# Optimization experiments

Hardware: AMD Instinct MI355X
Metric: run time of the kernel (lower is better)

The kernel has to match this reference:

```python
import jax, jax.numpy as jnp
import numpy as np

N_NODES = 50000
N_EDGES = 800000
N_REL = 6
N_LAYERS = 8
D = 256
NUM_GRAPHS = 512


def setup_inputs() -> dict:
    key = jax.random.key(0)
    ks = jax.random.split(key, 24)
    s = lambda *sh: 1.0 / np.sqrt(sh[0])
    inp = {
        "x": jax.random.normal(ks[0], (N_NODES, 13), dtype=jnp.float32),
        "edge_index": jax.random.randint(ks[1], (2, N_EDGES), 0, N_NODES, dtype=jnp.int64),
        "edge_type": jax.random.randint(ks[2], (N_EDGES,), 0, N_REL, dtype=jnp.int64),
        "batch": jnp.sort(jax.random.randint(ks[3], (N_NODES,), 0, NUM_GRAPHS, dtype=jnp.int64)),
        "enc_W": jax.random.normal(ks[4], (13, D), dtype=jnp.float32) * s(13),
        "enc_b": jnp.zeros((D,), dtype=jnp.float32),
        "prelu_a": jnp.float32(0.25),
        "rel_W": jax.random.normal(ks[5], (N_LAYERS, N_REL, D, D), dtype=jnp.float32) * s(D),
        "root_W": jax.random.normal(ks[6], (N_LAYERS, D, D), dtype=jnp.float32) * s(D),
        "conv_b": jnp.zeros((N_LAYERS, D), dtype=jnp.float32),
        "gp_W1": jax.random.normal(ks[7], (D, D), dtype=jnp.float32) * s(D),
        "gp_b1": jnp.zeros((D,), dtype=jnp.float32),
        "gp_W2": jax.random.normal(ks[8], (D, D), dtype=jnp.float32) * s(D),
        "gp_b2": jnp.zeros((D,), dtype=jnp.float32),
        "fc_W1": jax.random.normal(ks[9], (D, 1024), dtype=jnp.float32) * s(D),
        "fc_b1": jnp.zeros((1024,), dtype=jnp.float32),
        "fc_W2": jax.random.normal(ks[10], (1024, 512), dtype=jnp.float32) * s(1024),
        "fc_b2": jnp.zeros((512,), dtype=jnp.float32),
        "out_W": jax.random.normal(ks[11], (512, 1), dtype=jnp.float32) * s(512),
        "out_b": jnp.zeros((1,), dtype=jnp.float32),
    }
    return inp


def reference(x, edge_index, edge_type, batch, enc_W, enc_b, prelu_a, rel_W, root_W,
              conv_b, gp_W1, gp_b1, gp_W2, gp_b2, fc_W1, fc_b1, fc_W2, fc_b2, out_W, out_b):
    src, dst = edge_index[0], edge_index[1]
    h = x @ enc_W + enc_b  # [N, D]
    for i in range(N_LAYERS):
        skip = h
        # per-relation transform for all nodes: [R, N, D]
        xW = jnp.einsum('nd,rde->rne', h, rel_W[i])
        msgs = xW[edge_type, src]  # [E, D] gather by (relation, source node)
        agg = jax.ops.segment_sum(msgs, dst, num_segments=N_NODES)
        h = agg + h @ root_W[i] + conv_b[i]
        h = h + skip
        h = jnp.where(h > 0, h, prelu_a * h)  # PReLU (shared scalar)
        norm = jnp.sqrt(jnp.sum(h * h, axis=1, keepdims=True))
        h = h / jnp.maximum(norm, 1e-12)  # F.normalize(p=2, dim=1)
    g = jax.nn.relu(h @ gp_W1 + gp_b1) @ gp_W2 + gp_b2
    pooled = jax.ops.segment_sum(g, batch, num_segments=NUM_GRAPHS)  # global_add_pool
    z = jax.nn.relu(pooled @ fc_W1 + fc_b1)  # dropout = identity at eval
    z = jax.nn.relu(z @ fc_W2 + fc_b2)
    return jax.nn.relu(z @ out_W + out_b)  # [NUM_GRAPHS, 1]
```

## Files before the change

kernel.cpp:

```cpp
#include <hip/hip_runtime.h>

#define N_NODES   50000
#define N_EDGES   800000
#define N_REL     6
#define N_LAYERS  8
#define DD        256
#define NUM_GRAPHS 512

#define NKEYS      (N_REL * N_NODES)
#define SCAN_T     256
#define SCAN_E     8
#define SCAN_CHUNK (SCAN_T * SCAN_E)
#define SCAN_NB    ((NKEYS + SCAN_CHUNK - 1) / SCAN_CHUNK)

typedef _Float16 h4 __attribute__((ext_vector_type(4)));
typedef _Float16 h8 __attribute__((ext_vector_type(8)));
typedef float    f4 __attribute__((ext_vector_type(4)));

__device__ __forceinline__ void atomAddF(float* p, float v) { unsafeAtomicAdd(p, v); }

__device__ __forceinline__ void load_lds16(const void* g, void* l) {
    __builtin_amdgcn_global_load_lds(
        (const __attribute__((address_space(1))) uint32_t*)g,
        (__attribute__((address_space(3))) uint32_t*)l, 16, 0, 0);
}

__global__ __launch_bounds__(256) void enc_kernel(const float* __restrict__ x,
                                                  const float* __restrict__ W,
                                                  const float* __restrict__ b,
                                                  _Float16* __restrict__ Hhi,
                                                  _Float16* __restrict__ Hlo) {
    int n = blockIdx.x;
    int d = threadIdx.x;
    float s = b[d];
#pragma unroll
    for (int k = 0; k < 13; ++k) s = fmaf(x[n * 13 + k], W[k * 256 + d], s);
    const _Float16 hi = (_Float16)s;
    Hhi[(size_t)n * DD + d] = hi;
    Hlo[(size_t)n * DD + d] = (_Float16)(s - (float)hi);
}

__global__ __launch_bounds__(256) void wsplit_rel_kernel(const float* __restrict__ relW,
                                                         const float* __restrict__ rootW,
                                                         _Float16* __restrict__ wthi,
                                                         _Float16* __restrict__ wtlo) {
    const size_t id = (size_t)blockIdx.x * 256 + threadIdx.x;
    if (id >= (size_t)N_LAYERS * 7 * 256 * 256) return;
    const int k = (int)(id & 255);
    const int n = (int)((id >> 8) & 255);
    const int g = (int)((id >> 16) % 7);
    const int L = (int)((id >> 16) / 7);
    float w = (g < 6)
        ? relW[(((size_t)L * 6 + g) * 256 + k) * 256 + n]
        : rootW[((size_t)L * 256 + k) * 256 + n];
    if (g == 6 && k == n) w += 1.0f;
    const _Float16 hi = (_Float16)w;
    const size_t o = ((size_t)L * 256 + n) * 1792 + (size_t)g * 256 + k;
    wthi[o] = hi;
    wtlo[o] = (_Float16)(w - (float)hi);
}

__global__ __launch_bounds__(256) void wsplit_tr_kernel(const float* __restrict__ W,
                                                        _Float16* __restrict__ whi,
                                                        _Float16* __restrict__ wlo,
                                                        int K, int N) {
    const size_t id = (size_t)blockIdx.x * 256 + threadIdx.x;
    if (id >= (size_t)K * N) return;
    const int k = (int)(id % K), n = (int)(id / K);
    const float w = W[(size_t)k * N + n];
    const _Float16 hi = (_Float16)w;
    whi[(size_t)n * K + k] = hi;
    wlo[(size_t)n * K + k] = (_Float16)(w - (float)hi);
}

__global__ __launch_bounds__(256) void fsplit_kernel(const float* __restrict__ S,
                                                     _Float16* __restrict__ hi,
                                                     _Float16* __restrict__ lo, int total) {
    const int id = blockIdx.x * 256 + threadIdx.x;
    if (id >= total) return;
    const float v = S[id];
    const _Float16 h = (_Float16)v;
    hi[id] = h;
    lo[id] = (_Float16)(v - (float)h);
}

template <int MODE>
__global__ __launch_bounds__(256, 2) void gemm_lds(
    const _Float16* __restrict__ Ahi, const _Float16* __restrict__ Alo,
    const _Float16* __restrict__ Hhi, const _Float16* __restrict__ Hlo,
    const _Float16* __restrict__ Bhi, const _Float16* __restrict__ Blo,
    int lda, int ldb, int ldc, int boff_agg, int boff_h, int K_agg, int K_tot,
    float* __restrict__ Cf, _Float16* __restrict__ Ohi, _Float16* __restrict__ Olo,
    const float* __restrict__ bias, const float* __restrict__ pa, int M) {
    __shared__ _Float16 smem[24576];
    const int lane = threadIdx.x & 63;
    const int wave = threadIdx.x >> 6;
    const int lm = lane & 15, lq = lane >> 4;
    const int wm = wave & 1, wn = wave >> 1;
    const int mb = blockIdx.x * 128;
    const int nb = blockIdx.y * 256;

    f4 acc[4][8];
#pragma unroll
    for (int i = 0; i < 4; ++i)
#pragma unroll
        for (int j = 0; j < 8; ++j) acc[i][j] = (f4){0.f, 0.f, 0.f, 0.f};

    for (int k0 = 0; k0 < K_tot; k0 += 32) {
        const _Float16 *pAh, *pAl;
        int acol, bcol;
        if (k0 < K_agg) {
            const size_t pb = (size_t)(k0 >> 8) * (size_t)N_NODES * DD;
            pAh = Ahi + pb; pAl = Alo + pb;
            acol = k0 & 255;
            bcol = boff_agg + k0;
        } else {
            pAh = Hhi; pAl = Hlo;
            acol = k0 - K_agg;
            bcol = boff_h + (k0 - K_agg);
        }

        __syncthreads();
#pragma unroll
        for (int q = 0; q < 12; ++q) {
            const int ub = (q * 4 + wave) * 64;
            const int u  = ub + lane;
            const _Float16* gp;
            size_t ga;
            if (q < 4) {
                const int v = u & 511, row = v >> 2, slot = v & 3;
                const int c = slot ^ ((row >> 1) & 3);
                int rg = mb + row; if (rg >= M) rg = M - 1;
                gp = (q < 2) ? pAh : pAl;
                ga = (size_t)rg * lda + acol + c * 8;
            } else {
                const int v = u & 1023, row = v >> 2, slot = v & 3;
                const int c = slot ^ ((row >> 1) & 3);
                gp = (q < 8) ? Bhi : Blo;
                ga = (size_t)(nb + row) * ldb + bcol + c * 8;
            }
            load_lds16(gp + ga, smem + (size_t)ub * 8);
        }
        __syncthreads();

        h8 ah[4], al[4], bh[8], bl[8];
#pragma unroll
        for (int i = 0; i < 4; ++i) {
            const int row  = wm * 64 + i * 16 + lm;
            const int slot = lq ^ ((row >> 1) & 3);
            const int o    = (row * 4 + slot) * 8;
            ah[i] = *(const h8*)(smem + o);
            al[i] = *(const h8*)(smem + 4096 + o);
        }
#pragma unroll
        for (int j = 0; j < 8; ++j) {
            const int n    = wn * 128 + j * 16 + lm;
            const int slot = lq ^ ((n >> 1) & 3);
            const int o    = (n * 4 + slot) * 8;
            bh[j] = *(const h8*)(smem + 8192 + o);
            bl[j] = *(const h8*)(smem + 16384 + o);
        }
#pragma unroll
        for (int i = 0; i < 4; ++i)
#pragma unroll
            for (int j = 0; j < 8; ++j) {
                acc[i][j] = __builtin_amdgcn_mfma_f32_16x16x32_f16(ah[i], bh[j], acc[i][j], 0, 0, 0);
                acc[i][j] = __builtin_amdgcn_mfma_f32_16x16x32_f16(ah[i], bl[j], acc[i][j], 0, 0, 0);
                acc[i][j] = __builtin_amdgcn_mfma_f32_16x16x32_f16(al[i], bh[j], acc[i][j], 0, 0, 0);
            }
    }

    if (MODE == 0) {
#pragma unroll
        for (int i = 0; i < 4; ++i)
#pragma unroll
            for (int r = 0; r < 4; ++r) {
                const int row = mb + wm * 64 + i * 16 + lq * 4 + r;
                if (row >= M) continue;
#pragma unroll
                for (int j = 0; j < 8; ++j) {
                    const int col = nb + wn * 128 + j * 16 + lm;
                    Cf[(size_t)row * ldc + col] = acc[i][j][r] + bias[col];
                }
            }
    } else if (MODE == 3) {
#pragma unroll
        for (int i = 0; i < 4; ++i)
#pragma unroll
            for (int r = 0; r < 4; ++r) {
                const int row = mb + wm * 64 + i * 16 + lq * 4 + r;
                if (row >= M) continue;
#pragma unroll
                for (int j = 0; j < 8; ++j) {
                    const int col = nb + wn * 128 + j * 16 + lm;
                    Cf[(size_t)row * ldc + col] += acc[i][j][r];
                }
            }
    } else if (MODE == 2 || MODE == 4) {
#pragma unroll
        for (int i = 0; i < 4; ++i)
#pragma unroll
            for (int r = 0; r < 4; ++r) {
                const int row = mb + wm * 64 + i * 16 + lq * 4 + r;
                if (row >= M) continue;
#pragma unroll
                for (int j = 0; j < 8; ++j) {
                    const int col = nb + wn * 128 + j * 16 + lm;
                    float v = acc[i][j][r] + bias[col];
                    if (MODE == 2) v = fmaxf(v, 0.f);
                    const _Float16 hi = (_Float16)v;
                    const size_t idx = (size_t)row * ldc + col;
                    Ohi[idx] = hi;
                    Olo[idx] = (_Float16)(v - (float)hi);
                }
            }
    } else {
        float* shf = (float*)smem;
        const float a = pa[0];
        __syncthreads();
#pragma unroll
        for (int i = 0; i < 4; ++i)
#pragma unroll
            for (int r = 0; r < 4; ++r) {
                const int rl  = i * 16 + lq * 4 + r;
                const int row = mb + wm * 64 + rl;
                float rss = 0.f;
                if (row < M) {
#pragma unroll
                    for (int j = 0; j < 8; ++j) {
                        const int col = nb + wn * 128 + j * 16 + lm;
                        float v = acc[i][j][r] + Cf[(size_t)row * ldc + col];
                        v = v > 0.f ? v : a * v;
                        acc[i][j][r] = v;
                        rss = fmaf(v, v, rss);
                    }
                }
                rss += __shfl_xor(rss, 1, 64);
                rss += __shfl_xor(rss, 2, 64);
                rss += __shfl_xor(rss, 4, 64);
                rss += __shfl_xor(rss, 8, 64);
                if (lm == 0 && row < M) shf[wave * 64 + rl] = rss;
            }
        __syncthreads();
#pragma unroll
        for (int i = 0; i < 4; ++i)
#pragma unroll
            for (int r = 0; r < 4; ++r) {
                const int rl  = i * 16 + lq * 4 + r;
                const int row = mb + wm * 64 + rl;
                if (row >= M) continue;
                const float tot = shf[wm * 64 + rl] + shf[(2 + wm) * 64 + rl];
                const float inv = 1.0f / fmaxf(sqrtf(tot), 1e-12f);
#pragma unroll
                for (int j = 0; j < 8; ++j) {
                    const int col = nb + wn * 128 + j * 16 + lm;
                    const float v = acc[i][j][r] * inv;
                    const _Float16 hi = (_Float16)v;
                    const size_t idx = (size_t)row * ldc + col;
                    Ohi[idx] = hi;
                    Olo[idx] = (_Float16)(v - (float)hi);
                }
            }
    }
}

__global__ __launch_bounds__(256) void hist_kernel(const int* __restrict__ dst,
                                                   const int* __restrict__ etype,
                                                   int* __restrict__ cnt) {
    const int e = blockIdx.x * 256 + threadIdx.x;
    if (e >= N_EDGES) return;
    atomicAdd(&cnt[etype[e] * N_NODES + dst[e]], 1);
}

__global__ __launch_bounds__(SCAN_T) void scan1_kernel(const int* __restrict__ cnt,
                                                       int* __restrict__ off,
                                                       int* __restrict__ bsum) {
    __shared__ int sh[SCAN_T];
    const int b = blockIdx.x, t = threadIdx.x;
    const int base = b * SCAN_CHUNK + t * SCAN_E;
    int pre[SCAN_E];
    int s = 0;
#pragma unroll
    for (int i = 0; i < SCAN_E; ++i) {
        const int x = (base + i < NKEYS) ? cnt[base + i] : 0;
        pre[i] = s;
        s += x;
    }
    sh[t] = s;
    __syncthreads();
    for (int d = 1; d < SCAN_T; d <<= 1) {
        const int x = (t >= d) ? sh[t - d] : 0;
        __syncthreads();
        sh[t] += x;
        __syncthreads();
    }
    const int toff = (t == 0) ? 0 : sh[t - 1];
#pragma unroll
    for (int i = 0; i < SCAN_E; ++i)
        if (base + i < NKEYS) off[base + i] = toff + pre[i];
    if (t == SCAN_T - 1) bsum[b] = sh[SCAN_T - 1];
}

__global__ __launch_bounds__(SCAN_T) void scan2_kernel(int* __restrict__ bsum, int n) {
    __shared__ int sh[SCAN_T];
    const int t = threadIdx.x;
    const int base = t * SCAN_E;
    int pre[SCAN_E];
    int s = 0;
#pragma unroll
    for (int i = 0; i < SCAN_E; ++i) {
        const int x = (base + i < n) ? bsum[base + i] : 0;
        pre[i] = s;
        s += x;
    }
    sh[t] = s;
    __syncthreads();
    for (int d = 1; d < SCAN_T; d <<= 1) {
        const int x = (t >= d) ? sh[t - d] : 0;
        __syncthreads();
        sh[t] += x;
        __syncthreads();
    }
    const int toff = (t == 0) ? 0 : sh[t - 1];
#pragma unroll
    for (int i = 0; i < SCAN_E; ++i)
        if (base + i < n) bsum[base + i] = toff + pre[i];
}

__global__ __launch_bounds__(SCAN_T) void scan3_kernel(int* __restrict__ off,
                                                       const int* __restrict__ bsum) {
    const int b = blockIdx.x, t = threadIdx.x;
    const int add = bsum[b];
    const int base = b * SCAN_CHUNK + t * SCAN_E;
#pragma unroll
    for (int i = 0; i < SCAN_E; ++i)
        if (base + i < NKEYS) off[base + i] += add;
    if (b == 0 && t == 0) off[NKEYS] = N_EDGES;
}

__global__ __launch_bounds__(256) void csr_fill_kernel(const int* __restrict__ src,
                                                       const int* __restrict__ dst,
                                                       const int* __restrict__ etype,
                                                       int* __restrict__ cursor,
                                                       int* __restrict__ sorted_src) {
    const int e = blockIdx.x * 256 + threadIdx.x;
    if (e >= N_EDGES) return;
    const int key = etype[e] * N_NODES + dst[e];
    const int pos = atomicAdd(&cursor[key], 1);
    sorted_src[pos] = src[e];
}

__global__ __launch_bounds__(256) void agg_kernel(const _Float16* __restrict__ Hhi,
                                                  const _Float16* __restrict__ Hlo,
                                                  const int* __restrict__ off,
                                                  const int* __restrict__ isrc,
                                                  _Float16* __restrict__ agghi,
                                                  _Float16* __restrict__ agglo,
                                                  int rel0, int nrel) {
    const int p    = blockIdx.x * 4 + (threadIdx.x >> 6);
    const int lane = threadIdx.x & 63;
    const int half = lane >> 5, li = lane & 31;
    if (p >= nrel * N_NODES) return;
    const int pl   = p / N_NODES;
    const int node = p - pl * N_NODES;
    const int r    = rel0 + pl;
    const int s0 = off[r * N_NODES + node];
    const int s1 = off[r * N_NODES + node + 1];
    float a[8] = {0.f, 0.f, 0.f, 0.f, 0.f, 0.f, 0.f, 0.f};
    for (int e0 = s0; e0 < s1; e0 += 4) {
        const int ea = e0 + half;
        const int eb = e0 + 2 + half;
        const int sa = (ea < s1) ? isrc[ea] : -1;
        const int sb = (eb < s1) ? isrc[eb] : -1;
        if (sa >= 0) {
            const h8 vh = *(const h8*)(Hhi + (size_t)sa * DD + li * 8);
            const h8 vl = *(const h8*)(Hlo + (size_t)sa * DD + li * 8);
#pragma unroll
            for (int k = 0; k < 8; ++k) a[k] += (float)vh[k] + (float)vl[k];
        }
        if (sb >= 0) {
            const h8 vh = *(const h8*)(Hhi + (size_t)sb * DD + li * 8);
            const h8 vl = *(const h8*)(Hlo + (size_t)sb * DD + li * 8);
#pragma unroll
            for (int k = 0; k < 8; ++k) a[k] += (float)vh[k] + (float)vl[k];
        }
    }
#pragma unroll
    for (int k = 0; k < 8; ++k) a[k] += __shfl_xor(a[k], 32, 64);
    if (half == 0) {
        h8 oh, ol;
#pragma unroll
        for (int k = 0; k < 8; ++k) {
            oh[k] = (_Float16)a[k];
            ol[k] = (_Float16)(a[k] - (float)oh[k]);
        }
        const size_t o = ((size_t)pl * N_NODES + node) * DD + li * 8;
        *(h8*)(agghi + o) = oh;
        *(h8*)(agglo + o) = ol;
    }
}

__global__ __launch_bounds__(64) void pool_kernel(const _Float16* __restrict__ ghi,
                                                  const _Float16* __restrict__ glo,
                                                  const int* __restrict__ batch,
                                                  float* __restrict__ pooled) {
    const int c     = threadIdx.x;
    const int start = blockIdx.x * 128;
    const int end   = min(start + 128, N_NODES);
    int cur = batch[start];
    float4 acc = {0.f, 0.f, 0.f, 0.f};
    for (int n = start; n < end; ++n) {
        const int bn = batch[n];
        if (bn != cur) {
            float* p = pooled + (size_t)cur * DD + c * 4;
            atomAddF(p + 0, acc.x); atomAddF(p + 1, acc.y);
            atomAddF(p + 2, acc.z); atomAddF(p + 3, acc.w);
            acc = {0.f, 0.f, 0.f, 0.f};
            cur = bn;
        }
        const h4 vh = *(const h4*)(ghi + (size_t)n * DD + c * 4);
        const h4 vl = *(const h4*)(glo + (size_t)n * DD + c * 4);
        acc.x += (float)vh[0] + (float)vl[0];
        acc.y += (float)vh[1] + (float)vl[1];
        acc.z += (float)vh[2] + (float)vl[2];
        acc.w += (float)vh[3] + (float)vl[3];
    }
    float* p = pooled + (size_t)cur * DD + c * 4;
    atomAddF(p + 0, acc.x); atomAddF(p + 1, acc.y);
    atomAddF(p + 2, acc.z); atomAddF(p + 3, acc.w);
}

__global__ __launch_bounds__(64) void out_kernel(const _Float16* __restrict__ z2hi,
                                                 const _Float16* __restrict__ z2lo,
                                                 const float* __restrict__ W,
                                                 const float* __restrict__ b,
                                                 float* __restrict__ out) {
    const int g = blockIdx.x;
    const int t = threadIdx.x;
    float s = 0.f;
#pragma unroll
    for (int j = 0; j < 8; ++j) {
        const int idx = t + 64 * j;
        const float z = (float)z2hi[(size_t)g * 512 + idx] + (float)z2lo[(size_t)g * 512 + idx];
        s = fmaf(z, W[idx], s);
    }
#pragma unroll
    for (int off = 32; off; off >>= 1) s += __shfl_xor(s, off, 64);
    if (t == 0) {
        const float v = s + b[0];
        out[g] = v > 0.f ? v : 0.f;
    }
}

extern "C" void kernel_launch(void* const* d_in, const int* in_sizes, int n_in,
                              void* d_out, int out_size, void* d_ws, size_t ws_size,
                              hipStream_t stream) {
    const float* x       = (const float*)d_in[0];
    const int*   eidx    = (const int*)d_in[1];
    const int*   etype   = (const int*)d_in[2];
    const int*   batch   = (const int*)d_in[3];
    const float* enc_W   = (const float*)d_in[4];
    const float* enc_b   = (const float*)d_in[5];
    const float* prelu_a = (const float*)d_in[6];
    const float* rel_W   = (const float*)d_in[7];
    const float* root_W  = (const float*)d_in[8];
    const float* conv_b  = (const float*)d_in[9];
    const float* gp_W1   = (const float*)d_in[10];
    const float* gp_b1   = (const float*)d_in[11];
    const float* gp_W2   = (const float*)d_in[12];
    const float* gp_b2   = (const float*)d_in[13];
    const float* fc_W1   = (const float*)d_in[14];
    const float* fc_b1   = (const float*)d_in[15];
    const float* fc_W2   = (const float*)d_in[16];
    const float* fc_b2   = (const float*)d_in[17];
    const float* out_W   = (const float*)d_in[18];
    const float* out_b   = (const float*)d_in[19];
    float* out = (float*)d_out;

    uint8_t* wp = (uint8_t*)d_ws;
    auto alloc = [&](size_t bytes) {
        void* r = (void*)wp;
        wp += (bytes + 255) & ~(size_t)255;
        return r;
    };
    float*    base   = (float*)alloc((size_t)N_NODES * DD * 4);
    _Float16* Hhi    = (_Float16*)alloc((size_t)N_NODES * DD * 2);
    _Float16* Hlo    = (_Float16*)alloc((size_t)N_NODES * DD * 2);
    _Float16* agghi  = (_Float16*)alloc((size_t)2 * N_NODES * DD * 2);
    _Float16* agglo  = (_Float16*)alloc((size_t)2 * N_NODES * DD * 2);
    _Float16* wthi   = (_Float16*)alloc((size_t)N_LAYERS * 256 * 1792 * 2);
    _Float16* wtlo   = (_Float16*)alloc((size_t)N_LAYERS * 256 * 1792 * 2);
    _Float16* wtg1hi = (_Float16*)alloc((size_t)256 * 256 * 2);
    _Float16* wtg1lo = (_Float16*)alloc((size_t)256 * 256 * 2);
    _Float16* wtg2hi = (_Float16*)alloc((size_t)256 * 256 * 2);
    _Float16* wtg2lo = (_Float16*)alloc((size_t)256 * 256 * 2);
    _Float16* wtf1hi = (_Float16*)alloc((size_t)1024 * 256 * 2);
    _Float16* wtf1lo = (_Float16*)alloc((size_t)1024 * 256 * 2);
    _Float16* wtf2hi = (_Float16*)alloc((size_t)512 * 1024 * 2);
    _Float16* wtf2lo = (_Float16*)alloc((size_t)512 * 1024 * 2);
    float*    pooled = (float*)alloc((size_t)NUM_GRAPHS * DD * 4);
    _Float16* phi    = (_Float16*)alloc((size_t)NUM_GRAPHS * DD * 2);
    _Float16* plo    = (_Float16*)alloc((size_t)NUM_GRAPHS * DD * 2);
    _Float16* z1hi   = (_Float16*)alloc((size_t)NUM_GRAPHS * 1024 * 2);
    _Float16* z1lo   = (_Float16*)alloc((size_t)NUM_GRAPHS * 1024 * 2);
    _Float16* z2hi   = (_Float16*)alloc((size_t)NUM_GRAPHS * 512 * 2);
    _Float16* z2lo   = (_Float16*)alloc((size_t)NUM_GRAPHS * 512 * 2);
    int*      ioff   = (int*)alloc((size_t)(NKEYS + 1) * 4);
    int*      icur   = (int*)alloc((size_t)NKEYS * 4);
    int*      ibsum  = (int*)alloc(256 * 4);
    int*      isrc   = (int*)alloc((size_t)N_EDGES * 4);

    const int* src = eidx;
    const int* dst = eidx + N_EDGES;

    const size_t wtot = (size_t)N_LAYERS * 7 * 256 * 256;
    wsplit_rel_kernel<<<(int)((wtot + 255) / 256), 256, 0, stream>>>(rel_W, root_W, wthi, wtlo);
    wsplit_tr_kernel<<<256, 256, 0, stream>>>(gp_W1, wtg1hi, wtg1lo, 256, 256);
    wsplit_tr_kernel<<<256, 256, 0, stream>>>(gp_W2, wtg2hi, wtg2lo, 256, 256);
    wsplit_tr_kernel<<<1024, 256, 0, stream>>>(fc_W1, wtf1hi, wtf1lo, 256, 1024);
    wsplit_tr_kernel<<<2048, 256, 0, stream>>>(fc_W2, wtf2hi, wtf2lo, 1024, 512);

    hipMemsetAsync(icur, 0, (size_t)NKEYS * sizeof(int), stream);
    const int eb = (N_EDGES + 255) / 256;
    hist_kernel<<<eb, 256, 0, stream>>>(dst, etype, icur);
    scan1_kernel<<<SCAN_NB, SCAN_T, 0, stream>>>(icur, ioff, ibsum);
    scan2_kernel<<<1, SCAN_T, 0, stream>>>(ibsum, SCAN_NB);
    scan3_kernel<<<SCAN_NB, SCAN_T, 0, stream>>>(ioff, ibsum);
    hipMemcpyAsync(icur, ioff, (size_t)NKEYS * sizeof(int), hipMemcpyDeviceToDevice, stream);
    csr_fill_kernel<<<eb, 256, 0, stream>>>(src, dst, etype, icur, isrc);

    enc_kernel<<<N_NODES, 256, 0, stream>>>(x, enc_W, enc_b, Hhi, Hlo);

    const dim3 gG((N_NODES + 127) / 128, 1);
    const int  aggb = (2 * N_NODES + 3) / 4;

    for (int L = 0; L < N_LAYERS; ++L) {
        const _Float16* Bh = wthi + (size_t)L * 256 * 1792;
        const _Float16* Bl = wtlo + (size_t)L * 256 * 1792;
        agg_kernel<<<aggb, 256, 0, stream>>>(Hhi, Hlo, ioff, isrc, agghi, agglo, 0, 2);
        gemm_lds<0><<<gG, 256, 0, stream>>>(agghi, agglo, Hhi, Hlo, Bh, Bl,
                                            256, 1792, 256, 0, 1536, 512, 768,
                                            base, nullptr, nullptr,
                                            conv_b + L * DD, nullptr, N_NODES);
        agg_kernel<<<aggb, 256, 0, stream>>>(Hhi, Hlo, ioff, isrc, agghi, agglo, 2, 2);
        gemm_lds<3><<<gG, 256, 0, stream>>>(agghi, agglo, nullptr, nullptr, Bh, Bl,
                                            256, 1792, 256, 512, 0, 512, 512,
                                            base, nullptr, nullptr,
                                            nullptr, nullptr, N_NODES);
        agg_kernel<<<aggb, 256, 0, stream>>>(Hhi, Hlo, ioff, isrc, agghi, agglo, 4, 2);
        gemm_lds<1><<<gG, 256, 0, stream>>>(agghi, agglo, nullptr, nullptr, Bh, Bl,
                                            256, 1792, 256, 1024, 0, 512, 512,
                                            base, Hhi, Hlo,
                                            nullptr, prelu_a, N_NODES);
    }

    gemm_lds<2><<<gG, 256, 0, stream>>>(nullptr, nullptr, Hhi, Hlo, wtg1hi, wtg1lo,
                                        256, 256, 256, 0, 0, 0, 256,
                                        nullptr, agghi, agglo, gp_b1, nullptr, N_NODES);
    gemm_lds<4><<<gG, 256, 0, stream>>>(agghi, agglo, nullptr, nullptr, wtg2hi, wtg2lo,
                                        256, 256, 256, 0, 0, 256, 256,
                                        nullptr, agghi + (size_t)N_NODES * DD,
                                        agglo + (size_t)N_NODES * DD, gp_b2, nullptr, N_NODES);

    hipMemsetAsync(pooled, 0, (size_t)NUM_GRAPHS * DD * sizeof(float), stream);
    pool_kernel<<<(N_NODES + 127) / 128, 64, 0, stream>>>(
        agghi + (size_t)N_NODES * DD, agglo + (size_t)N_NODES * DD, batch, pooled);
    fsplit_kernel<<<(NUM_GRAPHS * DD + 255) / 256, 256, 0, stream>>>(
        pooled, phi, plo, NUM_GRAPHS * DD);

    gemm_lds<2><<<dim3(4, 4), 256, 0, stream>>>(nullptr, nullptr, phi, plo, wtf1hi, wtf1lo,
                                                256, 256, 1024, 0, 0, 0, 256,
                                                nullptr, z1hi, z1lo, fc_b1, nullptr,
                                                NUM_GRAPHS);
    gemm_lds<2><<<dim3(4, 2), 256, 0, stream>>>(nullptr, nullptr, z1hi, z1lo, wtf2hi, wtf2lo,
                                                1024, 1024, 512, 0, 0, 0, 1024,
                                                nullptr, z2hi, z2lo, fc_b2, nullptr,
                                                NUM_GRAPHS);
    out_kernel<<<NUM_GRAPHS, 64, 0, stream>>>(z2hi, z2lo, out_W, out_b, out);
}
```

Baseline: 3.225 ms.

## Fuse neighbor aggregation into per-layer GEMM kernel

Replaces the three aggregate-then-GEMM pairs per layer with a single layer kernel. Each block gathers relation-wise neighbor sums for its 128 nodes directly into shared memory, then runs the MFMA GEMM plus the PReLU/normalize epilogue. This removes the intermediate aggregation buffers, the fp32 partial-sum round trips and most launches. In exchange, the edge list is re-read for every 32-column chunk and the gathers are serialized per thread with no overlap against the matrix work.

```diff
diff --git a/kernel.cpp b/kernel.cpp
--- a/kernel.cpp
+++ b/kernel.cpp
@@ -84,14 +84,194 @@
     lo[id] = (_Float16)(v - (float)h);
 }
 
+__global__ __launch_bounds__(256, 2) void layer_kernel(
+    const _Float16* __restrict__ Hhi, const _Float16* __restrict__ Hlo,
+    const _Float16* __restrict__ Bhi, const _Float16* __restrict__ Blo,
+    const int* __restrict__ ioff, const int* __restrict__ isrc,
+    _Float16* __restrict__ Hnhi, _Float16* __restrict__ Hnlo,
+    const float* __restrict__ bias, const float* __restrict__ pa) {
+    __shared__ _Float16 smem[24576];
+    const int tid  = threadIdx.x;
+    const int lane = tid & 63;
+    const int wave = tid >> 6;
+    const int lm = lane & 15, lq = lane >> 4;
+    const int wm = wave & 1, wn = wave >> 1;
+    const int mb = blockIdx.x * 128;
+
+    const int nl   = tid >> 1;
+    const int half = tid & 1;
+    const int node = min(mb + nl, N_NODES - 1);
+
+    f4 acc[4][8];
+#pragma unroll
+    for (int i = 0; i < 4; ++i)
+#pragma unroll
+        for (int j = 0; j < 8; ++j) acc[i][j] = (f4){0.f, 0.f, 0.f, 0.f};
+
+    for (int seg = 0; seg < 7; ++seg) {
+        const bool isrel = (seg < 6);
+        int s0 = 0, s1 = 0;
+        if (isrel) {
+            s0 = ioff[seg * N_NODES + node];
+            s1 = ioff[seg * N_NODES + node + 1];
+        }
+#pragma unroll 1
+        for (int c8 = 0; c8 < 8; ++c8) {
+            const int acol = c8 * 32;
+            const int bcol = seg * 256 + acol;
+
+            __syncthreads();
+
+            if (isrel) {
+                float afp[16];
+#pragma unroll
+                for (int j = 0; j < 16; ++j) afp[j] = 0.f;
+                const int dbase = acol + half * 16;
+                for (int e = s0; e < s1; ++e) {
+                    const int s = isrc[e];
+                    const size_t hb = (size_t)s * DD + dbase;
+                    const h8 vh0 = *(const h8*)(Hhi + hb);
+                    const h8 vh1 = *(const h8*)(Hhi + hb + 8);
+                    const h8 vl0 = *(const h8*)(Hlo + hb);
+                    const h8 vl1 = *(const h8*)(Hlo + hb + 8);
+#pragma unroll
+                    for (int j = 0; j < 8; ++j) {
+                        afp[j]     += (float)vh0[j] + (float)vl0[j];
+                        afp[8 + j] += (float)vh1[j] + (float)vl1[j];
+                    }
+                }
+#pragma unroll
+                for (int u = 0; u < 2; ++u) {
+                    h8 oh, ol;
+#pragma unroll
+                    for (int j = 0; j < 8; ++j) {
+                        const float v = afp[u * 8 + j];
+                        oh[j] = (_Float16)v;
+                        ol[j] = (_Float16)(v - (float)oh[j]);
+                    }
+                    const int cc   = half * 2 + u;
+                    const int slot = cc ^ ((nl >> 1) & 3);
+                    const int o    = (nl * 4 + slot) * 8;
+                    *(h8*)(smem + o)        = oh;
+                    *(h8*)(smem + 4096 + o) = ol;
+                }
+#pragma unroll
+                for (int q = 4; q < 12; ++q) {
+                    const int ub = (q * 4 + wave) * 64;
+                    const int u  = (ub + lane) & 1023;
+                    const int row = u >> 2, slot = u & 3;
+                    const int cx = slot ^ ((row >> 1) & 3);
+                    const _Float16* gp = (q < 8) ? Bhi : Blo;
+                    const size_t gb = (size_t)row * 1792 + bcol + cx * 8;
+                    load_lds16(gp + gb, smem + (size_t)ub * 8);
+                }
+            } else {
+#pragma unroll
+                for (int q = 0; q < 12; ++q) {
+                    const int ub = (q * 4 + wave) * 64;
+                    const int u  = ub + lane;
+                    const _Float16* gp;
+                    size_t ga;
+                    if (q < 4) {
+                        const int v = u & 511, row = v >> 2, slot = v & 3;
+                        const int cx = slot ^ ((row >> 1) & 3);
+                        const int rg = min(mb + row, N_NODES - 1);
+                        gp = (q < 2) ? Hhi : Hlo;
+                        ga = (size_t)rg * DD + acol + cx * 8;
+                    } else {
+                        const int v = u & 1023, row = v >> 2, slot = v & 3;
+                        const int cx = slot ^ ((row >> 1) & 3);
+                        gp = (q < 8) ? Bhi : Blo;
+                        ga = (size_t)row * 1792 + bcol + cx * 8;
+                    }
+                    load_lds16(gp + ga, smem + (size_t)ub * 8);
+                }
+            }
+            __syncthreads();
+
+            h8 ah[4], al[4], bh[8], bl[8];
+#pragma unroll
+            for (int i = 0; i < 4; ++i) {
+                const int row  = wm * 64 + i * 16 + lm;
+                const int slot = lq ^ ((row >> 1) & 3);
+                const int o    = (row * 4 + slot) * 8;
+                ah[i] = *(const h8*)(smem + o);
+                al[i] = *(const h8*)(smem + 4096 + o);
+            }
+#pragma unroll
+            for (int j = 0; j < 8; ++j) {
+                const int n    = wn * 128 + j * 16 + lm;
+                const int slot = lq ^ ((n >> 1) & 3);
+                const int o    = (n * 4 + slot) * 8;
+                bh[j] = *(const h8*)(smem + 8192 + o);
+                bl[j] = *(const h8*)(smem + 16384 + o);
+            }
+#pragma unroll
+            for (int i = 0; i < 4; ++i)
+#pragma unroll
+                for (int j = 0; j < 8; ++j) {
+                    acc[i][j] = __builtin_amdgcn_mfma_f32_16x16x32_f16(ah[i], bh[j], acc[i][j], 0, 0, 0);
+                    acc[i][j] = __builtin_amdgcn_mfma_f32_16x16x32_f16(ah[i], bl[j], acc[i][j], 0, 0, 0);
+                    acc[i][j] = __builtin_amdgcn_mfma_f32_16x16x32_f16(al[i], bh[j], acc[i][j], 0, 0, 0);
+                }
+        }
+    }
+
+    float* shf = (float*)smem;
+    const float a = pa[0];
+    __syncthreads();
+#pragma unroll
+    for (int i = 0; i < 4; ++i)
+#pragma unroll
+        for (int r = 0; r < 4; ++r) {
+            const int rl  = i * 16 + lq * 4 + r;
+            const int row = mb + wm * 64 + rl;
+            float rss = 0.f;
+            if (row < N_NODES) {
+#pragma unroll
+                for (int j = 0; j < 8; ++j) {
+                    const int col = wn * 128 + j * 16 + lm;
+                    float v = acc[i][j][r] + bias[col];
+                    v = v > 0.f ? v : a * v;
+                    acc[i][j][r] = v;
+                    rss = fmaf(v, v, rss);
+                }
+            }
+            rss += __shfl_xor(rss, 1, 64);
+            rss += __shfl_xor(rss, 2, 64);
+            rss += __shfl_xor(rss, 4, 64);
+            rss += __shfl_xor(rss, 8, 64);
+            if (lm == 0 && row < N_NODES) shf[wave * 64 + rl] = rss;
+        }
+    __syncthreads();
+#pragma unroll
+    for (int i = 0; i < 4; ++i)
+#pragma unroll
+        for (int r = 0; r < 4; ++r) {
+            const int rl  = i * 16 + lq * 4 + r;
+            const int row = mb + wm * 64 + rl;
+            if (row >= N_NODES) continue;
+            const float tot = shf[wm * 64 + rl] + shf[(2 + wm) * 64 + rl];
+            const float inv = 1.0f / fmaxf(sqrtf(tot), 1e-12f);
+#pragma unroll
+            for (int j = 0; j < 8; ++j) {
+                const int col = wn * 128 + j * 16 + lm;
+                const float v = acc[i][j][r] * inv;
+                const _Float16 hi = (_Float16)v;
+                const size_t idx = (size_t)row * DD + col;
+                Hnhi[idx] = hi;
+                Hnlo[idx] = (_Float16)(v - (float)hi);
+            }
+        }
+}
+
 template <int MODE>
 __global__ __launch_bounds__(256, 2) void gemm_lds(
     const _Float16* __restrict__ Ahi, const _Float16* __restrict__ Alo,
-    const _Float16* __restrict__ Hhi, const _Float16* __restrict__ Hlo,
     const _Float16* __restrict__ Bhi, const _Float16* __restrict__ Blo,
-    int lda, int ldb, int ldc, int boff_agg, int boff_h, int K_agg, int K_tot,
-    float* __restrict__ Cf, _Float16* __restrict__ Ohi, _Float16* __restrict__ Olo,
-    const float* __restrict__ bias, const float* __restrict__ pa, int M) {
+    int lda, int ldb, int ldc, int K_tot,
+    _Float16* __restrict__ Ohi, _Float16* __restrict__ Olo,
+    const float* __restrict__ bias, int M) {
     __shared__ _Float16 smem[24576];
     const int lane = threadIdx.x & 63;
     const int wave = threadIdx.x >> 6;
@@ -107,19 +287,6 @@
         for (int j = 0; j < 8; ++j) acc[i][j] = (f4){0.f, 0.f, 0.f, 0.f};
 
     for (int k0 = 0; k0 < K_tot; k0 += 32) {
-        const _Float16 *pAh, *pAl;
-        int acol, bcol;
-        if (k0 < K_agg) {
-            const size_t pb = (size_t)(k0 >> 8) * (size_t)N_NODES * DD;
-            pAh = Ahi + pb; pAl = Alo + pb;
-            acol = k0 & 255;
-            bcol = boff_agg + k0;
-        } else {
-            pAh = Hhi; pAl = Hlo;
-            acol = k0 - K_agg;
-            bcol = boff_h + (k0 - K_agg);
-        }
-
         __syncthreads();
 #pragma unroll
         for (int q = 0; q < 12; ++q) {
@@ -129,15 +296,15 @@
             size_t ga;
             if (q < 4) {
                 const int v = u & 511, row = v >> 2, slot = v & 3;
-                const int c = slot ^ ((row >> 1) & 3);
-                int rg = mb + row; if (rg >= M) rg = M - 1;
-                gp = (q < 2) ? pAh : pAl;
-                ga = (size_t)rg * lda + acol + c * 8;
+                const int cx = slot ^ ((row >> 1) & 3);
+                const int rg = min(mb + row, M - 1);
+                gp = (q < 2) ? Ahi : Alo;
+                ga = (size_t)rg * lda + k0 + cx * 8;
             } else {
                 const int v = u & 1023, row = v >> 2, slot = v & 3;
-                const int c = slot ^ ((row >> 1) & 3);
+                const int cx = slot ^ ((row >> 1) & 3);
                 gp = (q < 8) ? Bhi : Blo;
-                ga = (size_t)(nb + row) * ldb + bcol + c * 8;
+                ga = (size_t)(nb + row) * ldb + k0 + cx * 8;
             }
             load_lds16(gp + ga, smem + (size_t)ub * 8);
         }
@@ -170,98 +337,23 @@
             }
     }
 
-    if (MODE == 0) {
-#pragma unroll
-        for (int i = 0; i < 4; ++i)
-#pragma unroll
-            for (int r = 0; r < 4; ++r) {
-                const int row = mb + wm * 64 + i * 16 + lq * 4 + r;
-                if (row >= M) continue;
-#pragma unroll
-                for (int j = 0; j < 8; ++j) {
-                    const int col = nb + wn * 128 + j * 16 + lm;
-                    Cf[(size_t)row * ldc + col] = acc[i][j][r] + bias[col];
-                }
-            }
-    } else if (MODE == 3) {
-#pragma unroll
-        for (int i = 0; i < 4; ++i)
-#pragma unroll
-            for (int r = 0; r < 4; ++r) {
-                const int row = mb + wm * 64 + i * 16 + lq * 4 + r;
-                if (row >= M) continue;
-#pragma unroll
-                for (int j = 0; j < 8; ++j) {
-                    const int col = nb + wn * 128 + j * 16 + lm;
-                    Cf[(size_t)row * ldc + col] += acc[i][j][r];
-                }
-            }
-    } else if (MODE == 2 || MODE == 4) {
-#pragma unroll
-        for (int i = 0; i < 4; ++i)
-#pragma unroll
-            for (int r = 0; r < 4; ++r) {
-                const int row = mb + wm * 64 + i * 16 + lq * 4 + r;
-                if (row >= M) continue;
-#pragma unroll
-                for (int j = 0; j < 8; ++j) {
-                    const int col = nb + wn * 128 + j * 16 + lm;
-                    float v = acc[i][j][r] + bias[col];
-                    if (MODE == 2) v = fmaxf(v, 0.f);
-                    const _Float16 hi = (_Float16)v;
-                    const size_t idx = (size_t)row * ldc + col;
-                    Ohi[idx] = hi;
-                    Olo[idx] = (_Float16)(v - (float)hi);
-                }
-            }
-    } else {
-        float* shf = (float*)smem;
-        const float a = pa[0];
-        __syncthreads();
-#pragma unroll
-        for (int i = 0; i < 4; ++i)
-#pragma unroll
-            for (int r = 0; r < 4; ++r) {
-                const int rl  = i * 16 + lq * 4 + r;
-                const int row = mb + wm * 64 + rl;
-                float rss = 0.f;
-                if (row < M) {
-#pragma unroll
-                    for (int j = 0; j < 8; ++j) {
-                        const int col = nb + wn * 128 + j * 16 + lm;
-                        float v = acc[i][j][r] + Cf[(size_t)row * ldc + col];
-                        v = v > 0.f ? v : a * v;
-                        acc[i][j][r] = v;
-                        rss = fmaf(v, v, rss);
-                    }
-                }
-                rss += __shfl_xor(rss, 1, 64);
-                rss += __shfl_xor(rss, 2, 64);
-                rss += __shfl_xor(rss, 4, 64);
-                rss += __shfl_xor(rss, 8, 64);
-                if (lm == 0 && row < M) shf[wave * 64 + rl] = rss;
-            }
-        __syncthreads();
-#pragma unroll
-        for (int i = 0; i < 4; ++i)
-#pragma unroll
-            for (int r = 0; r < 4; ++r) {
-                const int rl  = i * 16 + lq * 4 + r;
-                const int row = mb + wm * 64 + rl;
-                if (row >= M) continue;
-                const float tot = shf[wm * 64 + rl] + shf[(2 + wm) * 64 + rl];
-                const float inv = 1.0f / fmaxf(sqrtf(tot), 1e-12f);
-#pragma unroll
-                for (int j = 0; j < 8; ++j) {
-                    const int col = nb + wn * 128 + j * 16 + lm;
-                    const float v = acc[i][j][r] * inv;
-                    const _Float16 hi = (_Float16)v;
-                    const size_t idx = (size_t)row * ldc + col;
-                    Ohi[idx] = hi;
-                    Olo[idx] = (_Float16)(v - (float)hi);
-                }
-            }
-    }
+#pragma unroll
+    for (int i = 0; i < 4; ++i)
+#pragma unroll
+        for (int r = 0; r < 4; ++r) {
+            const int row = mb + wm * 64 + i * 16 + lq * 4 + r;
+            if (row >= M) continue;
+#pragma unroll
+            for (int j = 0; j < 8; ++j) {
+                const int col = nb + wn * 128 + j * 16 + lm;
+                float v = acc[i][j][r] + bias[col];
+                if (MODE == 2) v = fmaxf(v, 0.f);
+                const _Float16 hi = (_Float16)v;
+                const size_t idx = (size_t)row * ldc + col;
+                Ohi[idx] = hi;
+                Olo[idx] = (_Float16)(v - (float)hi);
+            }
+        }
 }
 
 __global__ __launch_bounds__(256) void hist_kernel(const int* __restrict__ dst,
@@ -348,56 +440,6 @@
     const int key = etype[e] * N_NODES + dst[e];
     const int pos = atomicAdd(&cursor[key], 1);
     sorted_src[pos] = src[e];
-}
-
-__global__ __launch_bounds__(256) void agg_kernel(const _Float16* __restrict__ Hhi,
-                                                  const _Float16* __restrict__ Hlo,
-                                                  const int* __restrict__ off,
-                                                  const int* __restrict__ isrc,
-                                                  _Float16* __restrict__ agghi,
-                                                  _Float16* __restrict__ agglo,
-                                                  int rel0, int nrel) {
-    const int p    = blockIdx.x * 4 + (threadIdx.x >> 6);
-    const int lane = threadIdx.x & 63;
-    const int half = lane >> 5, li = lane & 31;
-    if (p >= nrel * N_NODES) return;
-    const int pl   = p / N_NODES;
-    const int node = p - pl * N_NODES;
-    const int r    = rel0 + pl;
-    const int s0 = off[r * N_NODES + node];
-    const int s1 = off[r * N_NODES + node + 1];
-    float a[8] = {0.f, 0.f, 0.f, 0.f, 0.f, 0.f, 0.f, 0.f};
-    for (int e0 = s0; e0 < s1; e0 += 4) {
-        const int ea = e0 + half;
-        const int eb = e0 + 2 + half;
-        const int sa = (ea < s1) ? isrc[ea] : -1;
-        const int sb = (eb < s1) ? isrc[eb] : -1;
-        if (sa >= 0) {
-            const h8 vh = *(const h8*)(Hhi + (size_t)sa * DD + li * 8);
-            const h8 vl = *(const h8*)(Hlo + (size_t)sa * DD + li * 8);
-#pragma unroll
-            for (int k = 0; k < 8; ++k) a[k] += (float)vh[k] + (float)vl[k];
-        }
-        if (sb >= 0) {
-            const h8 vh = *(const h8*)(Hhi + (size_t)sb * DD + li * 8);
-            const h8 vl = *(const h8*)(Hlo + (size_t)sb * DD + li * 8);
-#pragma unroll
-            for (int k = 0; k < 8; ++k) a[k] += (float)vh[k] + (float)vl[k];
-        }
-    }
-#pragma unroll
-    for (int k = 0; k < 8; ++k) a[k] += __shfl_xor(a[k], 32, 64);
-    if (half == 0) {
-        h8 oh, ol;
-#pragma unroll
-        for (int k = 0; k < 8; ++k) {
-            oh[k] = (_Float16)a[k];
-            ol[k] = (_Float16)(a[k] - (float)oh[k]);
-        }
-        const size_t o = ((size_t)pl * N_NODES + node) * DD + li * 8;
-        *(h8*)(agghi + o) = oh;
-        *(h8*)(agglo + o) = ol;
-    }
 }
 
 __global__ __launch_bounds__(64) void pool_kernel(const _Float16* __restrict__ ghi,
@@ -483,11 +525,12 @@
         wp += (bytes + 255) & ~(size_t)255;
         return r;
     };
-    float*    base   = (float*)alloc((size_t)N_NODES * DD * 4);
-    _Float16* Hhi    = (_Float16*)alloc((size_t)N_NODES * DD * 2);
-    _Float16* Hlo    = (_Float16*)alloc((size_t)N_NODES * DD * 2);
-    _Float16* agghi  = (_Float16*)alloc((size_t)2 * N_NODES * DD * 2);
-    _Float16* agglo  = (_Float16*)alloc((size_t)2 * N_NODES * DD * 2);
+    _Float16* H0hi   = (_Float16*)alloc((size_t)N_NODES * DD * 2);
+    _Float16* H0lo   = (_Float16*)alloc((size_t)N_NODES * DD * 2);
+    _Float16* H1hi   = (_Float16*)alloc((size_t)N_NODES * DD * 2);
+    _Float16* H1lo   = (_Float16*)alloc((size_t)N_NODES * DD * 2);
+    _Float16* g2hi   = (_Float16*)alloc((size_t)N_NODES * DD * 2);
+    _Float16* g2lo   = (_Float16*)alloc((size_t)N_NODES * DD * 2);
     _Float16* wthi   = (_Float16*)alloc((size_t)N_LAYERS * 256 * 1792 * 2);
     _Float16* wtlo   = (_Float16*)alloc((size_t)N_LAYERS * 256 * 1792 * 2);
     _Float16* wtg1hi = (_Float16*)alloc((size_t)256 * 256 * 2);
@@ -529,52 +572,37 @@
     hipMemcpyAsync(icur, ioff, (size_t)NKEYS * sizeof(int), hipMemcpyDeviceToDevice, stream);
     csr_fill_kernel<<<eb, 256, 0, stream>>>(src, dst, etype, icur, isrc);
 
-    enc_kernel<<<N_NODES, 256, 0, stream>>>(x, enc_W, enc_b, Hhi, Hlo);
-
-    const dim3 gG((N_NODES + 127) / 128, 1);
-    const int  aggb = (2 * N_NODES + 3) / 4;
-
+    enc_kernel<<<N_NODES, 256, 0, stream>>>(x, enc_W, enc_b, H0hi, H0lo);
+
+    const int gB = (N_NODES + 127) / 128;
+    _Float16 *curhi = H0hi, *curlo = H0lo, *nxthi = H1hi, *nxtlo = H1lo;
     for (int L = 0; L < N_LAYERS; ++L) {
-        const _Float16* Bh = wthi + (size_t)L * 256 * 1792;
-        const _Float16* Bl = wtlo + (size_t)L * 256 * 1792;
-        agg_kernel<<<aggb, 256, 0, stream>>>(Hhi, Hlo, ioff, isrc, agghi, agglo, 0, 2);
-        gemm_lds<0><<<gG, 256, 0, stream>>>(agghi, agglo, Hhi, Hlo, Bh, Bl,
-                                            256, 1792, 256, 0, 1536, 512, 768,
-                                            base, nullptr, nullptr,
-                                            conv_b + L * DD, nullptr, N_NODES);
-        agg_kernel<<<aggb, 256, 0, stream>>>(Hhi, Hlo, ioff, isrc, agghi, agglo, 2, 2);
-        gemm_lds<3><<<gG, 256, 0, stream>>>(agghi, agglo, nullptr, nullptr, Bh, Bl,
-                                            256, 1792, 256, 512, 0, 512, 512,
-                                            base, nullptr, nullptr,
-                                            nullptr, nullptr, N_NODES);
-        agg_kernel<<<aggb, 256, 0, stream>>>(Hhi, Hlo, ioff, isrc, agghi, agglo, 4, 2);
-        gemm_lds<1><<<gG, 256, 0, stream>>>(agghi, agglo, nullptr, nullptr, Bh, Bl,
-                                            256, 1792, 256, 1024, 0, 512, 512,
-                                            base, Hhi, Hlo,
-                                            nullptr, prelu_a, N_NODES);
-    }
-
-    gemm_lds<2><<<gG, 256, 0, stream>>>(nullptr, nullptr, Hhi, Hlo, wtg1hi, wtg1lo,
-                                        256, 256, 256, 0, 0, 0, 256,
-                                        nullptr, agghi, agglo, gp_b1, nullptr, N_NODES);
-    gemm_lds<4><<<gG, 256, 0, stream>>>(agghi, agglo, nullptr, nullptr, wtg2hi, wtg2lo,
-                                        256, 256, 256, 0, 0, 256, 256,
-                                        nullptr, agghi + (size_t)N_NODES * DD,
-                                        agglo + (size_t)N_NODES * DD, gp_b2, nullptr, N_NODES);
+        layer_kernel<<<gB, 256, 0, stream>>>(
+            curhi, curlo,
+            wthi + (size_t)L * 256 * 1792, wtlo + (size_t)L * 256 * 1792,
+            ioff, isrc, nxthi, nxtlo, conv_b + L * DD, prelu_a);
+        _Float16* t;
+        t = curhi; curhi = nxthi; nxthi = t;
+        t = curlo; curlo = nxtlo; nxtlo = t;
+    }
+
+    gemm_lds<2><<<dim3(gB, 1), 256, 0, stream>>>(curhi, curlo, wtg1hi, wtg1lo,
+                                                 256, 256, 256, 256,
+                                                 nxthi, nxtlo, gp_b1, N_NODES);
+    gemm_lds<4><<<dim3(gB, 1), 256, 0, stream>>>(nxthi, nxtlo, wtg2hi, wtg2lo,
+                                                 256, 256, 256, 256,
+                                                 g2hi, g2lo, gp_b2, N_NODES);
 
     hipMemsetAsync(pooled, 0, (size_t)NUM_GRAPHS * DD * sizeof(float), stream);
-    pool_kernel<<<(N_NODES + 127) / 128, 64, 0, stream>>>(
-        agghi + (size_t)N_NODES * DD, agglo + (size_t)N_NODES * DD, batch, pooled);
+    pool_kernel<<<(N_NODES + 127) / 128, 64, 0, stream>>>(g2hi, g2lo, batch, pooled);
     fsplit_kernel<<<(NUM_GRAPHS * DD + 255) / 256, 256, 0, stream>>>(
         pooled, phi, plo, NUM_GRAPHS * DD);
 
-    gemm_lds<2><<<dim3(4, 4), 256, 0, stream>>>(nullptr, nullptr, phi, plo, wtf1hi, wtf1lo,
-                                                256, 256, 1024, 0, 0, 0, 256,
-                                                nullptr, z1hi, z1lo, fc_b1, nullptr,
-                                                NUM_GRAPHS);
-    gemm_lds<2><<<dim3(4, 2), 256, 0, stream>>>(nullptr, nullptr, z1hi, z1lo, wtf2hi, wtf2lo,
-                                                1024, 1024, 512, 0, 0, 0, 1024,
-                                                nullptr, z2hi, z2lo, fc_b2, nullptr,
-                                                NUM_GRAPHS);
+    gemm_lds<2><<<dim3(4, 4), 256, 0, stream>>>(phi, plo, wtf1hi, wtf1lo,
+                                                256, 256, 1024, 256,
+                                                z1hi, z1lo, fc_b1, NUM_GRAPHS);
+    gemm_lds<2><<<dim3(4, 2), 256, 0, stream>>>(z1hi, z1lo, wtf2hi, wtf2lo,
+                                                1024, 1024, 512, 1024,
+                                                z2hi, z2lo, fc_b2, NUM_GRAPHS);
     out_kernel<<<NUM_GRAPHS, 64, 0, stream>>>(z2hi, z2lo, out_W, out_b, out);
 }
```

New measurement: 3.965 ms. 1.23x slower.
